# Optimization experiments

Hardware: AMD Instinct MI355X
Metric: run time of the kernel (lower is better)

## Reference

```python
import jax, jax.numpy as jnp
import numpy as np
from jax import lax

STORAGE = 8
HIDDEN_HEAD = 32
N_BLOCKS = 16


def _conv(x, w, b, padding):
    # x: NCHW, w: OIHW
    y = lax.conv_general_dilated(
        x, w, window_strides=(1, 1), padding=padding,
        dimension_numbers=("NCHW", "OIHW", "NCHW"))
    return y + b[None, :, None, None]


def _min_pool3(x):
    # 3x3 sliding-window min, stride 1, same padding (pad value +inf so it
    return lax.reduce_window(x, float("inf"), lax.min,
                             (1, 1, 3, 3), (1, 1, 1, 1), "SAME")


def setup_inputs() -> dict:
    key = jax.random.key(0)
    ks = jax.random.split(key, 7)
    B, H, W = 8, 512, 512
    x = jax.random.normal(ks[0], (B, 1, H, W), dtype=jnp.float32)
    # initial 1x1 conv: 1 -> 8
    w0 = jax.random.normal(ks[1], (STORAGE, 1, 1, 1), dtype=jnp.float32) * 1.0
    b0 = jax.random.normal(ks[2], (STORAGE,), dtype=jnp.float32) * 0.1
    # head conv 3x3: 8 -> 32
    w1 = jax.random.normal(ks[3], (HIDDEN_HEAD, STORAGE, 3, 3), dtype=jnp.float32) * (1.0 / np.sqrt(STORAGE * 9))
    b1 = jax.random.normal(ks[4], (HIDDEN_HEAD,), dtype=jnp.float32) * 0.1
    # head conv 1x1: 32 -> 1
    w2 = jax.random.normal(ks[5], (1, HIDDEN_HEAD, 1, 1), dtype=jnp.float32) * (1.0 / np.sqrt(HIDDEN_HEAD))
    b2 = jax.random.normal(ks[6], (1,), dtype=jnp.float32) * 0.1
    return {"x": x, "w0": w0, "b0": b0, "w1": w1, "b1": b1, "w2": w2, "b2": b2}


def reference(x, w0, b0, w1, b1, w2, b2):
    h = _conv(x, w0, b0, "SAME")  # [B,8,H,W]
    for _ in range(N_BLOCKS):
        h = h + _min_pool3(h)
    h = _conv(h, w1, b1, "SAME")  # [B,32,H,W]
    h = jax.nn.relu(h)
    return _conv(h, w2, b2, "SAME")  # [B,1,H,W]
```

## Files before the change

### kernel.cpp

```cpp
#include <hip/hip_runtime.h>
#include <math.h>


#define N_PIX (512*512)
#define INF __builtin_inff()

typedef __attribute__((ext_vector_type(2))) float f2;

__device__ __forceinline__ unsigned long long f2bits(f2 v) {
    union { f2 f; unsigned long long u; } c; c.f = v; return c.u;
}
__device__ __forceinline__ f2 bits2f(unsigned long long u) {
    union { f2 f; unsigned long long u; } c; c.u = u; return c.f;
}

__device__ __forceinline__ float dpp_shr1(float v, float fill) {
    return __int_as_float(__builtin_amdgcn_update_dpp(
        __float_as_int(fill), __float_as_int(v), 0x138, 0xF, 0xF, false));
}
__device__ __forceinline__ float dpp_shl1(float v, float fill) {
    return __int_as_float(__builtin_amdgcn_update_dpp(
        __float_as_int(fill), __float_as_int(v), 0x130, 0xF, 0xF, false));
}
__device__ __forceinline__ float vmin3(float a, float b, float c) {
    float d;
    asm("v_min3_f32 %0, %1, %2, %3" : "=v"(d) : "v"(a), "v"(b), "v"(c));
    return d;
}

__device__ __forceinline__ void pkfma_P(f2& acc, unsigned long long w, f2 pq) {
    unsigned long long a = f2bits(acc), p = f2bits(pq);
    asm("v_pk_fma_f32 %0, %1, %2, %0 op_sel:[0,0,0] op_sel_hi:[1,0,1]"
        : "+v"(a) : "s"(w), "v"(p));
    acc = bits2f(a);
}
__device__ __forceinline__ void pkfma_Q(f2& acc, unsigned long long w, f2 pq) {
    unsigned long long a = f2bits(acc), p = f2bits(pq);
    asm("v_pk_fma_f32 %0, %1, %2, %0 op_sel:[0,1,0] op_sel_hi:[1,1,1]"
        : "+v"(a) : "s"(w), "v"(p));
    acc = bits2f(a);
}
__device__ __forceinline__ void pkmul_P(f2& acc, unsigned long long w, f2 pq) {
    unsigned long long a, p = f2bits(pq);
    asm("v_pk_mul_f32 %0, %1, %2 op_sel:[0,0] op_sel_hi:[1,0]"
        : "=v"(a) : "s"(w), "v"(p));
    acc = bits2f(a);
}

struct Row8 { float4 a, b; };

__device__ __forceinline__ Row8 row_update8(const Row8 up, const Row8 mid, const Row8 dn)
{
    float v0 = vmin3(up.a.x, mid.a.x, dn.a.x);
    float v1 = vmin3(up.a.y, mid.a.y, dn.a.y);
    float v2 = vmin3(up.a.z, mid.a.z, dn.a.z);
    float v3 = vmin3(up.a.w, mid.a.w, dn.a.w);
    float v4 = vmin3(up.b.x, mid.b.x, dn.b.x);
    float v5 = vmin3(up.b.y, mid.b.y, dn.b.y);
    float v6 = vmin3(up.b.z, mid.b.z, dn.b.z);
    float v7 = vmin3(up.b.w, mid.b.w, dn.b.w);
    float vmL = dpp_shr1(v7, INF);
    float vmR = dpp_shl1(v0, INF);
    Row8 o;
    o.a.x = mid.a.x + vmin3(vmL, v0, v1);
    o.a.y = mid.a.y + vmin3(v0, v1, v2);
    o.a.z = mid.a.z + vmin3(v1, v2, v3);
    o.a.w = mid.a.w + vmin3(v2, v3, v4);
    o.b.x = mid.b.x + vmin3(v3, v4, v5);
    o.b.y = mid.b.y + vmin3(v4, v5, v6);
    o.b.z = mid.b.z + vmin3(v5, v6, v7);
    o.b.w = mid.b.w + vmin3(v6, v7, vmR);
    return o;
}

__device__ __forceinline__ void halo_write(float* hp, int f0, int f1, const Row8& v) {
    *(float4*)(hp + f0) = v.a;
    *(float4*)(hp + f1) = v.b;
}
__device__ __forceinline__ Row8 halo_read(const float* hp, int f0, int f1) {
    Row8 v;
    v.a = *(const float4*)(hp + f0);
    v.b = *(const float4*)(hp + f1);
    return v;
}

__global__ __launch_bounds__(512, 2) void erode16_kernel(
    const float* __restrict__ x, float* __restrict__ A,
    const float* __restrict__ w0, const float* __restrict__ b0,
    const float* __restrict__ w1, const float* __restrict__ b1,
    const float* __restrict__ w2, float* __restrict__ W)
{
    if (blockIdx.x == 0 && blockIdx.y == 0 && threadIdx.x < 288) {
        int tid = threadIdx.x;
        int oc = tid / 9, k = tid - oc*9;
        int o = oc >> 1, hf = oc & 1;
        float wp = 0.f, wq = 0.f;
        for (int ic = 0; ic < 8; ++ic) {
            float a = w0[ic];
            float w = w1[oc*72 + ic*9 + k];
            if (a > 0.f) wp += w * a;
            else         wq += w * (-a);
        }
        W[(o*9 + k)*2 + hf]       = wp;
        W[288 + (o*9 + k)*2 + hf] = wq;
        if (k == 0) {
            float beta[9];
            for (int kk = 0; kk < 9; ++kk) {
                float s = 0.f;
                for (int ic = 0; ic < 8; ++ic) s += b0[ic] * w1[oc*72 + ic*9 + kk];
                beta[kk] = 65536.0f * s;
            }
            float R[3], Lb[3], Rr[3];
            for (int r = 0; r < 3; ++r) {
                R[r]  = beta[r*3] + beta[r*3+1] + beta[r*3+2];
                Lb[r] = beta[r*3 + 0];
                Rr[r] = beta[r*3 + 2];
            }
            float bb = b1[oc];
            float Dv[3]  = { bb + R[1] + R[2], bb + R[0] + R[1] + R[2], bb + R[0] + R[1] };
            float ELv[3] = { Lb[1] + Lb[2], Lb[0] + Lb[1] + Lb[2], Lb[0] + Lb[1] };
            float ERv[3] = { Rr[1] + Rr[2], Rr[0] + Rr[1] + Rr[2], Rr[0] + Rr[1] };
            for (int c = 0; c < 3; ++c) {
                W[576 + c*32 + o*2 + hf] = Dv[c];
                W[672 + c*32 + o*2 + hf] = ELv[c];
                W[768 + c*32 + o*2 + hf] = ERv[c];
            }
            W[864 + o*2 + hf] = w2[oc];
        }
    }

    __shared__ float halo[2][8][4][512];
    const int tid   = threadIdx.x;
    const int lane  = tid & 63;
    const int w     = tid >> 6;
    const int ty    = blockIdx.x;
    const int plane = blockIdx.y;
    const int colg  = lane * 8;
    const int row0g = ty*32 - 16 + w*8;

    const int f0 = (lane*8)     ^ (lane & 4);
    const int f1 = (lane*8 + 4) ^ (lane & 4);

    const int wS = __builtin_amdgcn_readfirstlane(w);
    const bool edge_band = (wS == 0) || (wS == 7);

    const float* sp = x + (plane & 7)*N_PIX;
    const float sgn = (plane >= 8) ? -1.f : 1.f;

    Row8 h[8];
    #pragma unroll
    for (int r = 0; r < 8; ++r) {
        int gy = row0g + r;
        if ((unsigned)gy < 512u) {
            const float* rp = sp + gy*512 + colg;
            float4 a = *(const float4*)rp;
            float4 b = *(const float4*)(rp + 4);
            h[r].a = make_float4(a.x*sgn, a.y*sgn, a.z*sgn, a.w*sgn);
            h[r].b = make_float4(b.x*sgn, b.y*sgn, b.z*sgn, b.w*sgn);
        } else {
            h[r].a = make_float4(INF, INF, INF, INF);
            h[r].b = h[r].a;
        }
    }

    const Row8 inf8 = { make_float4(INF,INF,INF,INF), make_float4(INF,INF,INF,INF) };
    for (int s = 0; s < 8; ++s) {
        int par = s & 1;
        if (edge_band && s >= 4) { __syncthreads(); continue; }
        halo_write(&halo[par][w][0][0], f0, f1, h[0]);
        halo_write(&halo[par][w][1][0], f0, f1, h[1]);
        halo_write(&halo[par][w][2][0], f0, f1, h[6]);
        halo_write(&halo[par][w][3][0], f0, f1, h[7]);
        Row8 n2 = row_update8(h[1], h[2], h[3]);
        Row8 n3 = row_update8(h[2], h[3], h[4]);
        Row8 n4 = row_update8(h[3], h[4], h[5]);
        Row8 n5 = row_update8(h[4], h[5], h[6]);
        __syncthreads();
        Row8 um2 = inf8, um1 = inf8, dp0 = inf8, dp1 = inf8;
        if (w > 0) {
            um2 = halo_read(&halo[par][w-1][2][0], f0, f1);
            um1 = halo_read(&halo[par][w-1][3][0], f0, f1);
        }
        if (w < 7) {
            dp0 = halo_read(&halo[par][w+1][0][0], f0, f1);
            dp1 = halo_read(&halo[par][w+1][1][0], f0, f1);
        }
        Row8 nm1 = row_update8(um2, um1, h[0]);
        Row8 n0  = row_update8(um1, h[0], h[1]);
        Row8 n1  = row_update8(h[0], h[1], h[2]);
        Row8 n6  = row_update8(h[5], h[6], h[7]);
        Row8 n7  = row_update8(h[6], h[7], dp0);
        Row8 n8  = row_update8(h[7], dp0, dp1);
        h[0] = row_update8(nm1, n0, n1);
        h[1] = row_update8(n0,  n1, n2);
        h[2] = row_update8(n1,  n2, n3);
        h[3] = row_update8(n2,  n3, n4);
        h[4] = row_update8(n3,  n4, n5);
        h[5] = row_update8(n4,  n5, n6);
        h[6] = row_update8(n5,  n6, n7);
        h[7] = row_update8(n6,  n7, n8);
    }

    if (w >= 2 && w <= 5) {
        float* dp = A + plane*N_PIX;
        #pragma unroll
        for (int r = 0; r < 8; ++r) {
            float* op = dp + (row0g + r)*512 + colg;
            *(float4*)op       = h[r].a;
            *(float4*)(op + 4) = h[r].b;
        }
    }
}

__global__ __launch_bounds__(256) void head_kernel(
    const float* __restrict__ A, const float* __restrict__ W,
    const float* __restrict__ b2, float* __restrict__ out)
{
    const int tid  = threadIdx.x;
    const int lane = tid & 63;
    const int w    = tid >> 6;
    const int img  = blockIdx.x >> 7;
    const int y    = (blockIdx.x & 127)*4 + w;
    const int x0   = lane*8;

    const float* P = A + img*N_PIX;
    const float* Q = A + (8 + img)*N_PIX;

    f2 pq[3][10];
    #pragma unroll
    for (int dy = 0; dy < 3; ++dy) {
        int gy = y + dy - 1;
        if ((unsigned)gy < 512u) {
            const float* rp = P + gy*512 + x0;
            const float* rq = Q + gy*512 + x0;
            float4 a = *(const float4*)rp;
            float4 b = *(const float4*)(rp + 4);
            float4 c = *(const float4*)rq;
            float4 d = *(const float4*)(rq + 4);
            pq[dy][1] = (f2){a.x, c.x}; pq[dy][2] = (f2){a.y, c.y};
            pq[dy][3] = (f2){a.z, c.z}; pq[dy][4] = (f2){a.w, c.w};
            pq[dy][5] = (f2){b.x, d.x}; pq[dy][6] = (f2){b.y, d.y};
            pq[dy][7] = (f2){b.z, d.z}; pq[dy][8] = (f2){b.w, d.w};
            pq[dy][0] = (f2){dpp_shr1(b.w, 0.f), dpp_shr1(d.w, 0.f)};
            pq[dy][9] = (f2){dpp_shl1(a.x, 0.f), dpp_shl1(c.x, 0.f)};
        } else {
            #pragma unroll
            for (int j = 0; j < 10; ++j) pq[dy][j] = (f2){0.f, 0.f};
        }
    }

    const int wcase = (y == 0) ? 0 : ((y == 511) ? 2 : 1);
    const unsigned long long* WPv = (const unsigned long long*)W;
    const unsigned long long* WQv = (const unsigned long long*)(W + 288);
    const f2* Dpv  = (const f2*)(W + 576 + wcase*32);
    const f2* ELv  = (const f2*)(W + 672 + wcase*32);
    const f2* ERv  = (const f2*)(W + 768 + wcase*32);
    const f2* w2v  = (const f2*)(W + 864);
    const float mLs = (lane == 0)  ? -1.f : 0.f;
    const float mRs = (lane == 63) ? -1.f : 0.f;
    const f2 mLp = (f2){mLs, mLs};
    const f2 mRp = (f2){mRs, mRs};

    f2 opk[8];
    #pragma unroll
    for (int j = 0; j < 8; ++j) opk[j] = (f2){0.f, 0.f};

    #pragma unroll 2
    for (int o = 0; o < 16; ++o) {
        f2 acc[8];
        {
            unsigned long long wv = WPv[o*9];
            #pragma unroll
            for (int j = 0; j < 8; ++j) pkmul_P(acc[j], wv, pq[0][j]);
        }
        #pragma unroll
        for (int t = 1; t < 9; ++t) {
            const int ky = t / 3, kx = t - ky*3;
            unsigned long long wv = WPv[o*9 + t];
            #pragma unroll
            for (int j = 0; j < 8; ++j) pkfma_P(acc[j], wv, pq[ky][kx + j]);
        }
        #pragma unroll
        for (int t = 0; t < 9; ++t) {
            const int ky = t / 3, kx = t - ky*3;
            unsigned long long wv = WQv[o*9 + t];
            #pragma unroll
            for (int j = 0; j < 8; ++j) pkfma_Q(acc[j], wv, pq[ky][kx + j]);
        }
        f2 bp = Dpv[o];
        #pragma unroll
        for (int j = 0; j < 8; ++j) acc[j] += bp;
        acc[0] += ELv[o] * mLp;
        acc[7] += ERv[o] * mRp;
        f2 sc = w2v[o];
        #pragma unroll
        for (int j = 0; j < 8; ++j) {
            acc[j].x = fmaxf(acc[j].x, 0.f);
            acc[j].y = fmaxf(acc[j].y, 0.f);
            opk[j] += acc[j] * sc;
        }
    }

    float bb = b2[0];
    float o0 = opk[0].x + opk[0].y + bb, o1 = opk[1].x + opk[1].y + bb;
    float o2 = opk[2].x + opk[2].y + bb, o3 = opk[3].x + opk[3].y + bb;
    float o4 = opk[4].x + opk[4].y + bb, o5 = opk[5].x + opk[5].y + bb;
    float o6 = opk[6].x + opk[6].y + bb, o7 = opk[7].x + opk[7].y + bb;
    float* op = out + img*N_PIX + y*512 + x0;
    *(float4*)(op)     = make_float4(o0, o1, o2, o3);
    *(float4*)(op + 4) = make_float4(o4, o5, o6, o7);
}

extern "C" void kernel_launch(void* const* d_in, const int* in_sizes, int n_in,
                              void* d_out, int out_size, void* d_ws, size_t ws_size,
                              hipStream_t stream) {
    const float* x  = (const float*)d_in[0];
    const float* w0 = (const float*)d_in[1];
    const float* b0 = (const float*)d_in[2];
    const float* w1 = (const float*)d_in[3];
    const float* b1 = (const float*)d_in[4];
    const float* w2 = (const float*)d_in[5];
    const float* b2 = (const float*)d_in[6];
    float* out = (float*)d_out;

    float* wsf = (float*)d_ws;
    float* A = wsf;
    float* W = wsf + 16*N_PIX;

    dim3 eg(16, 16);
    erode16_kernel<<<eg, 512, 0, stream>>>(x, A, w0, b0, w1, b1, w2, W);

    head_kernel<<<1024, 256, 0, stream>>>(A, W, b2, out);
}
```

Before: 122.8 us.

## Fuse erosion and head kernels into one cooperative launch with grid sync

Merges the erosion kernel and the conv head kernel into a single cooperative kernel, with a threadfence and grid-wide sync between the phases. After the sync, each 512-thread block computes two output rows per wave for its assigned image and row range. This removes a kernel launch and its gap. In exchange, the head runs on 256 blocks of 512 threads instead of 1024 blocks of 256, under the erosion kernel's launch bounds. That may lower occupancy or hurt register allocation, and the grid barrier adds its own cost.

```diff
diff --git a/kernel.cpp b/kernel.cpp
--- a/kernel.cpp
+++ b/kernel.cpp
@@ -1,9 +1,12 @@
 #include <hip/hip_runtime.h>
+#include <hip/hip_cooperative_groups.h>
 #include <math.h>
 
 
 #define N_PIX (512*512)
 #define INF __builtin_inff()
+
+namespace cg = cooperative_groups;
 
 typedef __attribute__((ext_vector_type(2))) float f2;
 
@@ -84,11 +87,104 @@
     return v;
 }
 
-__global__ __launch_bounds__(512, 2) void erode16_kernel(
+__device__ __forceinline__ void head_row(
+    const float* __restrict__ A, const float* __restrict__ W,
+    float bb, float* __restrict__ out, int img, int y, int lane)
+{
+    const int x0 = lane*8;
+    const float* P = A + img*N_PIX;
+    const float* Q = A + (8 + img)*N_PIX;
+
+    f2 pq[3][10];
+    #pragma unroll
+    for (int dy = 0; dy < 3; ++dy) {
+        int gy = y + dy - 1;
+        if ((unsigned)gy < 512u) {
+            const float* rp = P + gy*512 + x0;
+            const float* rq = Q + gy*512 + x0;
+            float4 a = *(const float4*)rp;
+            float4 b = *(const float4*)(rp + 4);
+            float4 c = *(const float4*)rq;
+            float4 d = *(const float4*)(rq + 4);
+            pq[dy][1] = (f2){a.x, c.x}; pq[dy][2] = (f2){a.y, c.y};
+            pq[dy][3] = (f2){a.z, c.z}; pq[dy][4] = (f2){a.w, c.w};
+            pq[dy][5] = (f2){b.x, d.x}; pq[dy][6] = (f2){b.y, d.y};
+            pq[dy][7] = (f2){b.z, d.z}; pq[dy][8] = (f2){b.w, d.w};
+            pq[dy][0] = (f2){dpp_shr1(b.w, 0.f), dpp_shr1(d.w, 0.f)};
+            pq[dy][9] = (f2){dpp_shl1(a.x, 0.f), dpp_shl1(c.x, 0.f)};
+        } else {
+            #pragma unroll
+            for (int j = 0; j < 10; ++j) pq[dy][j] = (f2){0.f, 0.f};
+        }
+    }
+
+    const int wcase = (y == 0) ? 0 : ((y == 511) ? 2 : 1);
+    const unsigned long long* WPv = (const unsigned long long*)W;
+    const unsigned long long* WQv = (const unsigned long long*)(W + 288);
+    const f2* Dpv  = (const f2*)(W + 576 + wcase*32);
+    const f2* ELv  = (const f2*)(W + 672 + wcase*32);
+    const f2* ERv  = (const f2*)(W + 768 + wcase*32);
+    const f2* w2v  = (const f2*)(W + 864);
+    const float mLs = (lane == 0)  ? -1.f : 0.f;
+    const float mRs = (lane == 63) ? -1.f : 0.f;
+    const f2 mLp = (f2){mLs, mLs};
+    const f2 mRp = (f2){mRs, mRs};
+
+    f2 opk[8];
+    #pragma unroll
+    for (int j = 0; j < 8; ++j) opk[j] = (f2){0.f, 0.f};
+
+    #pragma unroll 2
+    for (int o = 0; o < 16; ++o) {
+        f2 acc[8];
+        {
+            unsigned long long wv = WPv[o*9];
+            #pragma unroll
+            for (int j = 0; j < 8; ++j) pkmul_P(acc[j], wv, pq[0][j]);
+        }
+        #pragma unroll
+        for (int t = 1; t < 9; ++t) {
+            const int ky = t / 3, kx = t - ky*3;
+            unsigned long long wv = WPv[o*9 + t];
+            #pragma unroll
+            for (int j = 0; j < 8; ++j) pkfma_P(acc[j], wv, pq[ky][kx + j]);
+        }
+        #pragma unroll
+        for (int t = 0; t < 9; ++t) {
+            const int ky = t / 3, kx = t - ky*3;
+            unsigned long long wv = WQv[o*9 + t];
+            #pragma unroll
+            for (int j = 0; j < 8; ++j) pkfma_Q(acc[j], wv, pq[ky][kx + j]);
+        }
+        f2 bp = Dpv[o];
+        #pragma unroll
+        for (int j = 0; j < 8; ++j) acc[j] += bp;
+        acc[0] += ELv[o] * mLp;
+        acc[7] += ERv[o] * mRp;
+        f2 sc = w2v[o];
+        #pragma unroll
+        for (int j = 0; j < 8; ++j) {
+            acc[j].x = fmaxf(acc[j].x, 0.f);
+            acc[j].y = fmaxf(acc[j].y, 0.f);
+            opk[j] += acc[j] * sc;
+        }
+    }
+
+    float o0 = opk[0].x + opk[0].y + bb, o1 = opk[1].x + opk[1].y + bb;
+    float o2 = opk[2].x + opk[2].y + bb, o3 = opk[3].x + opk[3].y + bb;
+    float o4 = opk[4].x + opk[4].y + bb, o5 = opk[5].x + opk[5].y + bb;
+    float o6 = opk[6].x + opk[6].y + bb, o7 = opk[7].x + opk[7].y + bb;
+    float* op = out + img*N_PIX + y*512 + x0;
+    *(float4*)(op)     = make_float4(o0, o1, o2, o3);
+    *(float4*)(op + 4) = make_float4(o4, o5, o6, o7);
+}
+
+__global__ __launch_bounds__(512, 2) void sdf_fused_kernel(
     const float* __restrict__ x, float* __restrict__ A,
     const float* __restrict__ w0, const float* __restrict__ b0,
     const float* __restrict__ w1, const float* __restrict__ b1,
-    const float* __restrict__ w2, float* __restrict__ W)
+    const float* __restrict__ w2, const float* __restrict__ b2,
+    float* __restrict__ W, float* __restrict__ out)
 {
     if (blockIdx.x == 0 && blockIdx.y == 0 && threadIdx.x < 288) {
         int tid = threadIdx.x;
@@ -210,105 +306,18 @@
             *(float4*)(op + 4) = h[r].b;
         }
     }
-}
-
-__global__ __launch_bounds__(256) void head_kernel(
-    const float* __restrict__ A, const float* __restrict__ W,
-    const float* __restrict__ b2, float* __restrict__ out)
-{
-    const int tid  = threadIdx.x;
-    const int lane = tid & 63;
-    const int w    = tid >> 6;
-    const int img  = blockIdx.x >> 7;
-    const int y    = (blockIdx.x & 127)*4 + w;
-    const int x0   = lane*8;
-
-    const float* P = A + img*N_PIX;
-    const float* Q = A + (8 + img)*N_PIX;
-
-    f2 pq[3][10];
+
+    __threadfence();
+    cg::this_grid().sync();
+
+    const int img   = plane & 7;
+    const int ybase = ty*32 + ((plane >= 8) ? 16 : 0);
+    const float bb  = b2[0];
     #pragma unroll
-    for (int dy = 0; dy < 3; ++dy) {
-        int gy = y + dy - 1;
-        if ((unsigned)gy < 512u) {
-            const float* rp = P + gy*512 + x0;
-            const float* rq = Q + gy*512 + x0;
-            float4 a = *(const float4*)rp;
-            float4 b = *(const float4*)(rp + 4);
-            float4 c = *(const float4*)rq;
-            float4 d = *(const float4*)(rq + 4);
-            pq[dy][1] = (f2){a.x, c.x}; pq[dy][2] = (f2){a.y, c.y};
-            pq[dy][3] = (f2){a.z, c.z}; pq[dy][4] = (f2){a.w, c.w};
-            pq[dy][5] = (f2){b.x, d.x}; pq[dy][6] = (f2){b.y, d.y};
-            pq[dy][7] = (f2){b.z, d.z}; pq[dy][8] = (f2){b.w, d.w};
-            pq[dy][0] = (f2){dpp_shr1(b.w, 0.f), dpp_shr1(d.w, 0.f)};
-            pq[dy][9] = (f2){dpp_shl1(a.x, 0.f), dpp_shl1(c.x, 0.f)};
-        } else {
-            #pragma unroll
-            for (int j = 0; j < 10; ++j) pq[dy][j] = (f2){0.f, 0.f};
-        }
-    }
-
-    const int wcase = (y == 0) ? 0 : ((y == 511) ? 2 : 1);
-    const unsigned long long* WPv = (const unsigned long long*)W;
-    const unsigned long long* WQv = (const unsigned long long*)(W + 288);
-    const f2* Dpv  = (const f2*)(W + 576 + wcase*32);
-    const f2* ELv  = (const f2*)(W + 672 + wcase*32);
-    const f2* ERv  = (const f2*)(W + 768 + wcase*32);
-    const f2* w2v  = (const f2*)(W + 864);
-    const float mLs = (lane == 0)  ? -1.f : 0.f;
-    const float mRs = (lane == 63) ? -1.f : 0.f;
-    const f2 mLp = (f2){mLs, mLs};
-    const f2 mRp = (f2){mRs, mRs};
-
-    f2 opk[8];
-    #pragma unroll
-    for (int j = 0; j < 8; ++j) opk[j] = (f2){0.f, 0.f};
-
-    #pragma unroll 2
-    for (int o = 0; o < 16; ++o) {
-        f2 acc[8];
-        {
-            unsigned long long wv = WPv[o*9];
-            #pragma unroll
-            for (int j = 0; j < 8; ++j) pkmul_P(acc[j], wv, pq[0][j]);
-        }
-        #pragma unroll
-        for (int t = 1; t < 9; ++t) {
-            const int ky = t / 3, kx = t - ky*3;
-            unsigned long long wv = WPv[o*9 + t];
-            #pragma unroll
-            for (int j = 0; j < 8; ++j) pkfma_P(acc[j], wv, pq[ky][kx + j]);
-        }
-        #pragma unroll
-        for (int t = 0; t < 9; ++t) {
-            const int ky = t / 3, kx = t - ky*3;
-            unsigned long long wv = WQv[o*9 + t];
-            #pragma unroll
-            for (int j = 0; j < 8; ++j) pkfma_Q(acc[j], wv, pq[ky][kx + j]);
-        }
-        f2 bp = Dpv[o];
-        #pragma unroll
-        for (int j = 0; j < 8; ++j) acc[j] += bp;
-        acc[0] += ELv[o] * mLp;
-        acc[7] += ERv[o] * mRp;
-        f2 sc = w2v[o];
-        #pragma unroll
-        for (int j = 0; j < 8; ++j) {
-            acc[j].x = fmaxf(acc[j].x, 0.f);
-            acc[j].y = fmaxf(acc[j].y, 0.f);
-            opk[j] += acc[j] * sc;
-        }
-    }
-
-    float bb = b2[0];
-    float o0 = opk[0].x + opk[0].y + bb, o1 = opk[1].x + opk[1].y + bb;
-    float o2 = opk[2].x + opk[2].y + bb, o3 = opk[3].x + opk[3].y + bb;
-    float o4 = opk[4].x + opk[4].y + bb, o5 = opk[5].x + opk[5].y + bb;
-    float o6 = opk[6].x + opk[6].y + bb, o7 = opk[7].x + opk[7].y + bb;
-    float* op = out + img*N_PIX + y*512 + x0;
-    *(float4*)(op)     = make_float4(o0, o1, o2, o3);
-    *(float4*)(op + 4) = make_float4(o4, o5, o6, o7);
+    for (int k = 0; k < 2; ++k) {
+        int y = ybase + w*2 + k;
+        head_row(A, W, bb, out, img, y, lane);
+    }
 }
 
 extern "C" void kernel_launch(void* const* d_in, const int* in_sizes, int n_in,
@@ -327,8 +336,8 @@
     float* A = wsf;
     float* W = wsf + 16*N_PIX;
 
-    dim3 eg(16, 16);
-    erode16_kernel<<<eg, 512, 0, stream>>>(x, A, w0, b0, w1, b1, w2, W);
-
-    head_kernel<<<1024, 256, 0, stream>>>(A, W, b2, out);
-}
+    void* args[] = { (void*)&x, (void*)&A, (void*)&w0, (void*)&b0, (void*)&w1,
+                     (void*)&b1, (void*)&w2, (void*)&b2, (void*)&W, (void*)&out };
+    hipLaunchCooperativeKernel((const void*)sdf_fused_kernel,
+                               dim3(16, 16), dim3(512), args, 0, stream);
+}
```

New measurement: 248.9 us. 103% more time.
